# Performance work log

Measured on AMD Instinct MI355X. Metric: run time of the kernel, lower is better.

## Reference

```python
import jax, jax.numpy as jnp
import numpy as np

D_MODEL = 2048
NUM_CLASSES = 50257
N_BASIS = 8
RANK = 4
HIDDEN = 128
SCALE = 1.0
LN_EPS = 1e-5


def setup_inputs() -> dict:
    key = jax.random.key(0)
    ks = jax.random.split(key, 12)
    B = 2048
    lim_base = 1.0 / np.sqrt(D_MODEL)
    lim_ctx = 1.0 / np.sqrt(D_MODEL)
    lim_coeff = 1.0 / np.sqrt(HIDDEN)
    basis_std = np.sqrt(2.0 / (D_MODEL + RANK))
    return {
        "x": jax.random.normal(ks[0], (B, D_MODEL), jnp.float32),
        "context": jax.random.normal(ks[1], (B, D_MODEL), jnp.float32),
        "base_w": jax.random.uniform(ks[2], (NUM_CLASSES, D_MODEL), jnp.float32, -lim_base, lim_base),
        "base_b": jax.random.uniform(ks[3], (NUM_CLASSES,), jnp.float32, -lim_base, lim_base),
        "ctx_w": jax.random.uniform(ks[4], (HIDDEN, D_MODEL), jnp.float32, -lim_ctx, lim_ctx),
        "ctx_b": jax.random.uniform(ks[5], (HIDDEN,), jnp.float32, -lim_ctx, lim_ctx),
        "ln_g": jnp.ones((HIDDEN,), jnp.float32),
        "ln_b": jnp.zeros((HIDDEN,), jnp.float32),
        "coeff_w": jax.random.uniform(ks[6], (N_BASIS, HIDDEN), jnp.float32, -lim_coeff, lim_coeff),
        "coeff_b": jax.random.uniform(ks[7], (N_BASIS,), jnp.float32, -lim_coeff, lim_coeff),
        "basis_A": jax.random.normal(ks[8], (N_BASIS, RANK, D_MODEL), jnp.float32) * basis_std,
        # original zero-inits basis_B; use small randn so the LoRA path is exercised
        "basis_B": jax.random.normal(ks[9], (N_BASIS, NUM_CLASSES, RANK), jnp.float32) * 0.02,
    }


def reference(x, context, base_w, base_b, ctx_w, ctx_b, ln_g, ln_b,
              coeff_w, coeff_b, basis_A, basis_B):
    # ctx MLP: linear -> LayerNorm -> GELU(exact) -> linear
    h0 = context @ ctx_w.T + ctx_b                       # (B, H)
    mu = jnp.mean(h0, axis=-1, keepdims=True)
    var = jnp.var(h0, axis=-1, keepdims=True)
    hn = (h0 - mu) * jax.lax.rsqrt(var + LN_EPS) * ln_g + ln_b
    h = jax.nn.gelu(hn, approximate=False)
    coeffs = h @ coeff_w.T + coeff_b                     # (B, n_basis)

    # per-sample LoRA without materializing (B, num_classes, rank) B-tensor
    # z_br = x_bd * (coeffs_bn basis_A_nrd)
    z = jnp.einsum('bd,bn,nrd->br', x, coeffs, basis_A)  # (B, rank)
    # delta_bc = z_br * (coeffs_bn basis_B_ncr)
    u = jnp.einsum('bn,br->bnr', coeffs, z).reshape(x.shape[0], N_BASIS * RANK)
    Bmat = jnp.transpose(basis_B, (0, 2, 1)).reshape(N_BASIS * RANK, NUM_CLASSES)
    delta = u @ Bmat                                     # (B, num_classes)

    return x @ base_w.T + base_b + SCALE * delta
```

## Files before the change

kernel.cpp:

```cpp
#include <hip/hip_runtime.h>
#include <cstdint>
#include <cstddef>

#define D_MODEL 2048
#define NUM_CLASSES 50257
#define N_PAD 50304
#define N_BASIS 8
#define RANK 4
#define HIDDEN 128
#define B_ROWS 2048
#define KE 2080
#define NTILES 6288
#define LN_EPS 1e-5f

typedef short short8 __attribute__((ext_vector_type(8)));
typedef float f32x4 __attribute__((ext_vector_type(4)));

__device__ __forceinline__ uint16_t f2bf(float f) {
    union { float f; uint32_t u; } c; c.f = f;
    uint32_t r = c.u + 0x7FFFu + ((c.u >> 16) & 1u);
    return (uint16_t)(r >> 16);
}

__device__ __forceinline__ short8 pack8(float4 a, float4 b) {
    union { short8 v; uint16_t u[8]; } p;
    p.u[0] = f2bf(a.x); p.u[1] = f2bf(a.y); p.u[2] = f2bf(a.z); p.u[3] = f2bf(a.w);
    p.u[4] = f2bf(b.x); p.u[5] = f2bf(b.y); p.u[6] = f2bf(b.z); p.u[7] = f2bf(b.w);
    return p.v;
}

__device__ __forceinline__ short8 zero8() {
    union { short8 s; uint16_t u[8]; } z;
    #pragma unroll
    for (int i = 0; i < 8; i++) z.u[i] = 0;
    return z.s;
}

__device__ __forceinline__ void async16(const void* g, void* l) {
    __builtin_amdgcn_global_load_lds(
        (const __attribute__((address_space(1))) unsigned int*)g,
        (__attribute__((address_space(3))) unsigned int*)l, 16, 0, 0);
}

__global__ void k_cvt_x(const float* __restrict__ x, uint16_t* __restrict__ Aext) {
    int chunk = blockIdx.x * 256 + threadIdx.x;
    int b = chunk >> 8, c8 = (chunk & 255) * 8;
    const float4* src = (const float4*)(x + (size_t)b * D_MODEL + c8);
    float4 f0 = src[0], f1 = src[1];
    *(short8*)(Aext + (size_t)b * KE + c8) = pack8(f0, f1);
}

__global__ void k_transpose(const float* __restrict__ src, float* __restrict__ dst,
                            int R, int C) {
    int i = blockIdx.x * 256 + threadIdx.x;
    if (i >= R * C) return;
    int c = i / R, r = i - c * R;
    dst[i] = src[(size_t)r * C + c];
}

__global__ void k_cvt_bw(const float* __restrict__ bw, const float* __restrict__ bB,
                         uint16_t* __restrict__ Bext) {
    int row = blockIdx.x;
    int c8 = threadIdx.x * 8;
    short8 v;
    if (row < NUM_CLASSES) {
        const float4* src = (const float4*)(bw + (size_t)row * D_MODEL + c8);
        v = pack8(src[0], src[1]);
    } else v = zero8();
    *(short8*)(Bext + (size_t)row * KE + c8) = v;
    if (threadIdx.x < 4) {
        int t = threadIdx.x;
        short8 e;
        if (row < NUM_CLASSES) {
            float4 v0 = *(const float4*)(bB + ((size_t)(2 * t)     * NUM_CLASSES + row) * RANK);
            float4 v1 = *(const float4*)(bB + ((size_t)(2 * t + 1) * NUM_CLASSES + row) * RANK);
            e = pack8(v0, v1);
        } else e = zero8();
        *(short8*)(Bext + (size_t)row * KE + D_MODEL + t * 8) = e;
    }
}

__global__ void k_cvt_bbt(const float* __restrict__ bB, uint16_t* __restrict__ dst,
                          int ld, int coloff) {
    int row = blockIdx.x * 256 + threadIdx.x;
    if (row >= N_PAD) return;
    union { short8 v[4]; uint16_t u[32]; } p;
    if (row < NUM_CLASSES) {
        #pragma unroll
        for (int nb = 0; nb < N_BASIS; nb++) {
            float4 v = *(const float4*)(bB + ((size_t)nb * NUM_CLASSES + row) * RANK);
            p.u[nb*4+0] = f2bf(v.x); p.u[nb*4+1] = f2bf(v.y);
            p.u[nb*4+2] = f2bf(v.z); p.u[nb*4+3] = f2bf(v.w);
        }
    } else {
        #pragma unroll
        for (int i = 0; i < 32; i++) p.u[i] = 0;
    }
    uint16_t* d = dst + (size_t)row * ld + coloff;
    #pragma unroll
    for (int i = 0; i < 4; i++) *(short8*)(d + i * 8) = p.v[i];
}

__global__ void k_ctx(const float* __restrict__ context, const float* __restrict__ ctx_wT,
                      const float* __restrict__ ctx_b, const float* __restrict__ ln_g,
                      const float* __restrict__ ln_b, const float* __restrict__ coeff_w,
                      const float* __restrict__ coeff_b, float* __restrict__ coeffs) {
    __shared__ float sctx[D_MODEL];
    __shared__ float s1[HIDDEN], s2[HIDDEN], sh[HIDDEN];
    int tid = threadIdx.x, b = blockIdx.x;
    const float4* csrc = (const float4*)(context + (size_t)b * D_MODEL);
    for (int i = tid; i < D_MODEL / 4; i += HIDDEN) ((float4*)sctx)[i] = csrc[i];
    __syncthreads();
    float a0 = 0.f, a1 = 0.f, a2 = 0.f, a3 = 0.f;
    #pragma unroll 4
    for (int k = 0; k < D_MODEL; k += 4) {
        a0 += ctx_wT[(size_t)(k + 0) * HIDDEN + tid] * sctx[k + 0];
        a1 += ctx_wT[(size_t)(k + 1) * HIDDEN + tid] * sctx[k + 1];
        a2 += ctx_wT[(size_t)(k + 2) * HIDDEN + tid] * sctx[k + 2];
        a3 += ctx_wT[(size_t)(k + 3) * HIDDEN + tid] * sctx[k + 3];
    }
    float h0 = (a0 + a1) + (a2 + a3) + ctx_b[tid];
    s1[tid] = h0; s2[tid] = h0 * h0;
    __syncthreads();
    for (int off = HIDDEN / 2; off > 0; off >>= 1) {
        if (tid < off) { s1[tid] += s1[tid + off]; s2[tid] += s2[tid + off]; }
        __syncthreads();
    }
    float mu  = s1[0] * (1.f / HIDDEN);
    float var = s2[0] * (1.f / HIDDEN) - mu * mu;
    float hn = (h0 - mu) * rsqrtf(var + LN_EPS) * ln_g[tid] + ln_b[tid];
    float h = 0.5f * hn * (1.f + erff(hn * 0.70710678118654752f));
    sh[tid] = h;
    __syncthreads();
    if (tid < N_BASIS) {
        const float* cw = coeff_w + tid * HIDDEN;
        float a = 0.f;
        #pragma unroll 4
        for (int k = 0; k < HIDDEN; k++) a += cw[k] * sh[k];
        coeffs[b * N_BASIS + tid] = a + coeff_b[tid];
    }
}

__global__ void k_zu(const float* __restrict__ x, const float* __restrict__ basis_AT,
                     const float* __restrict__ coeffs, uint16_t* __restrict__ Aext) {
    __shared__ float sx[D_MODEL];
    __shared__ float part[128];
    __shared__ float st[32];
    __shared__ float sz[RANK];
    int tid = threadIdx.x, b = blockIdx.x;
    const float4* xs = (const float4*)(x + (size_t)b * D_MODEL);
    for (int i = tid; i < D_MODEL / 4; i += 128) ((float4*)sx)[i] = xs[i];
    __syncthreads();
    int j = tid & 31, s = tid >> 5;
    int k0 = s * (D_MODEL / 4);
    float a0 = 0.f, a1 = 0.f, a2 = 0.f, a3 = 0.f;
    #pragma unroll 4
    for (int k = 0; k < D_MODEL / 4; k += 4) {
        a0 += basis_AT[(size_t)(k0 + k + 0) * 32 + j] * sx[k0 + k + 0];
        a1 += basis_AT[(size_t)(k0 + k + 1) * 32 + j] * sx[k0 + k + 1];
        a2 += basis_AT[(size_t)(k0 + k + 2) * 32 + j] * sx[k0 + k + 2];
        a3 += basis_AT[(size_t)(k0 + k + 3) * 32 + j] * sx[k0 + k + 3];
    }
    part[tid] = (a0 + a1) + (a2 + a3);
    __syncthreads();
    if (tid < 32) st[tid] = part[tid] + part[tid + 32] + part[tid + 64] + part[tid + 96];
    __syncthreads();
    if (tid < RANK) {
        float z = 0.f;
        #pragma unroll
        for (int nb = 0; nb < N_BASIS; nb++) z += coeffs[b * N_BASIS + nb] * st[nb * RANK + tid];
        sz[tid] = z;
    }
    __syncthreads();
    if (tid < 32) {
        int nb = tid >> 2, r = tid & 3;
        float u = coeffs[b * N_BASIS + nb] * sz[r];
        Aext[(size_t)b * KE + D_MODEL + tid] = f2bf(u);
    }
}

template<bool FULLB>
__global__ __launch_bounds__(256) void k_gemm(
        const uint16_t* __restrict__ Aext,
        const uint16_t* __restrict__ Bbuf,
        const float* __restrict__ bw,
        const float* __restrict__ base_b,
        float* __restrict__ out) {
    __shared__ uint16_t sA[2][128 * 32];
    __shared__ uint16_t sB[2][128 * 32];
    const int tid = threadIdx.x;
    const int lane = tid & 63, w = tid >> 6;
    const int l = blockIdx.x;
    const int tile = (l & 7) * (NTILES / 8) + (l >> 3);
    const int bm = tile & 15, bn = tile >> 4;
    const int wm = (w >> 1) * 64, wn = (w & 1) * 64;
    const int sr = tid >> 2, sc = (tid & 3) * 8;
    f32x4 acc[4][4] = {};

    const uint16_t* gA = Aext + (size_t)(bm * 128 + sr) * KE + sc;

    auto stageA = [&](int kk, int sel) {
        async16(gA + kk, &sA[sel][w * 512]);
        async16(gA + (size_t)64 * KE + kk, &sA[sel][2048 + w * 512]);
    };
    auto stageBfull = [&](int kk, int sel) {
        const uint16_t* gB = Bbuf + (size_t)(bn * 128 + sr) * KE + sc + kk;
        async16(gB, &sB[sel][w * 512]);
        async16(gB + (size_t)64 * KE, &sB[sel][2048 + w * 512]);
    };
    auto stageBfb = [&](int kk, int sel) {
        if (kk < D_MODEL) {
            #pragma unroll
            for (int it = 0; it < 2; it++) {
                int rr = it * 64 + sr;
                int gr = bn * 128 + rr;
                short8 v;
                if (gr < NUM_CLASSES) {
                    const float4* src = (const float4*)(bw + (size_t)gr * D_MODEL + kk + sc);
                    v = pack8(src[0], src[1]);
                } else v = zero8();
                *(short8*)(&sB[sel][rr * 32 + sc]) = v;
            }
        } else {
            #pragma unroll
            for (int it = 0; it < 2; it++) {
                int rr = it * 64 + sr;
                async16(Bbuf + (size_t)(bn * 128 + rr) * 32 + (kk - D_MODEL) + sc,
                        &sB[sel][it * 2048 + w * 512]);
            }
        }
    };

    stageA(0, 0);
    if constexpr (FULLB) stageBfull(0, 0); else stageBfb(0, 0);
    __syncthreads();

    int cur = 0;
    for (int kk = 0; kk < KE; kk += 32) {
        int nxt = cur ^ 1;
        if (kk + 32 < KE) {
            stageA(kk + 32, nxt);
            if constexpr (FULLB) stageBfull(kk + 32, nxt); else stageBfb(kk + 32, nxt);
        }
        const uint16_t* pA = sA[cur] + (lane >> 4) * 8;
        const uint16_t* pB = sB[cur] + (lane >> 4) * 8;
        short8 af[4], bfv[4];
        #pragma unroll
        for (int i = 0; i < 4; i++)
            af[i] = *(const short8*)(pA + (wm + i * 16 + (lane & 15)) * 32);
        #pragma unroll
        for (int j = 0; j < 4; j++)
            bfv[j] = *(const short8*)(pB + (wn + j * 16 + (lane & 15)) * 32);
        #pragma unroll
        for (int i = 0; i < 4; i++)
            #pragma unroll
            for (int j = 0; j < 4; j++)
                acc[i][j] = __builtin_amdgcn_mfma_f32_16x16x32_bf16(af[i], bfv[j], acc[i][j], 0, 0, 0);
        __syncthreads();
        cur = nxt;
    }

    const int rb = bm * 128 + wm + ((lane >> 4) << 2);
    const int cb = bn * 128 + wn + (lane & 15);
    #pragma unroll
    for (int j = 0; j < 4; j++) {
        int col = cb + j * 16;
        if (col < NUM_CLASSES) {
            float bias = base_b[col];
            #pragma unroll
            for (int i = 0; i < 4; i++) {
                int r0 = rb + i * 16;
                out[(size_t)(r0 + 0) * NUM_CLASSES + col] = acc[i][j][0] + bias;
                out[(size_t)(r0 + 1) * NUM_CLASSES + col] = acc[i][j][1] + bias;
                out[(size_t)(r0 + 2) * NUM_CLASSES + col] = acc[i][j][2] + bias;
                out[(size_t)(r0 + 3) * NUM_CLASSES + col] = acc[i][j][3] + bias;
            }
        }
    }
}

extern "C" void kernel_launch(void* const* d_in, const int* in_sizes, int n_in,
                              void* d_out, int out_size, void* d_ws, size_t ws_size,
                              hipStream_t stream) {
    const float* x       = (const float*)d_in[0];
    const float* context = (const float*)d_in[1];
    const float* base_w  = (const float*)d_in[2];
    const float* base_b  = (const float*)d_in[3];
    const float* ctx_w   = (const float*)d_in[4];
    const float* ctx_b   = (const float*)d_in[5];
    const float* ln_g    = (const float*)d_in[6];
    const float* ln_b    = (const float*)d_in[7];
    const float* coeff_w = (const float*)d_in[8];
    const float* coeff_b = (const float*)d_in[9];
    const float* basis_A = (const float*)d_in[10];
    const float* basis_B = (const float*)d_in[11];
    float* out = (float*)d_out;

    uint8_t* ws = (uint8_t*)d_ws;
    const size_t szA    = (size_t)B_ROWS * KE * 2;
    const size_t szCoef = (size_t)B_ROWS * N_BASIS * 4;
    const size_t szWT   = (size_t)D_MODEL * HIDDEN * 4;
    const size_t szAT   = (size_t)D_MODEL * 32 * 4;
    const size_t szBext = (size_t)N_PAD * KE * 2;
    const size_t base   = szA + szCoef + szWT + szAT;
    const bool full = ws_size >= base + szBext;

    uint16_t* Aext    = (uint16_t*)ws;
    float*    coeffs  = (float*)(ws + szA);
    float*    ctx_wT  = (float*)(ws + szA + szCoef);
    float*    basisAT = (float*)(ws + szA + szCoef + szWT);
    uint16_t* Bbuf    = (uint16_t*)(ws + base);

    k_cvt_x<<<2048, 256, 0, stream>>>(x, Aext);
    k_transpose<<<(HIDDEN * D_MODEL + 255) / 256, 256, 0, stream>>>(ctx_w, ctx_wT, HIDDEN, D_MODEL);
    k_transpose<<<(32 * D_MODEL + 255) / 256, 256, 0, stream>>>(basis_A, basisAT, 32, D_MODEL);
    if (full) {
        k_cvt_bw<<<N_PAD, 256, 0, stream>>>(base_w, basis_B, Bbuf);
    } else {
        k_cvt_bbt<<<(N_PAD + 255) / 256, 256, 0, stream>>>(basis_B, Bbuf, 32, 0);
    }
    k_ctx<<<2048, HIDDEN, 0, stream>>>(context, ctx_wT, ctx_b, ln_g, ln_b,
                                       coeff_w, coeff_b, coeffs);
    k_zu<<<2048, 128, 0, stream>>>(x, basisAT, coeffs, Aext);

    if (full) k_gemm<true ><<<NTILES, 256, 0, stream>>>(Aext, Bbuf, base_w, base_b, out);
    else      k_gemm<false><<<NTILES, 256, 0, stream>>>(Aext, Bbuf, base_w, base_b, out);
}
```

Before: 1.529 ms.

## Add 256x256-tile GEMM with swizzled LDS, 64-wide K steps and deeper prefetch

```diff
diff --git a/kernel.cpp b/kernel.cpp
--- a/kernel.cpp
+++ b/kernel.cpp
@@ -5,12 +5,17 @@
 #define D_MODEL 2048
 #define NUM_CLASSES 50257
 #define N_PAD 50304
+#define N_PAD2 50432
 #define N_BASIS 8
 #define RANK 4
 #define HIDDEN 128
 #define B_ROWS 2048
 #define KE 2080
+#define KP 2112
+#define KPB (KP*2)
+#define NTK 33
 #define NTILES 6288
+#define NT2 1576
 #define LN_EPS 1e-5f
 
 typedef short short8 __attribute__((ext_vector_type(8)));
@@ -42,12 +47,20 @@
         (__attribute__((address_space(3))) unsigned int*)l, 16, 0, 0);
 }
 
+__device__ __forceinline__ int swz(int q) { return q ^ (((q >> 9) & 1) << 5); }
+
+#define BARRIER() do { asm volatile("" ::: "memory"); \
+    __builtin_amdgcn_s_barrier(); asm volatile("" ::: "memory"); } while (0)
+
 __global__ void k_cvt_x(const float* __restrict__ x, uint16_t* __restrict__ Aext) {
     int chunk = blockIdx.x * 256 + threadIdx.x;
-    int b = chunk >> 8, c8 = (chunk & 255) * 8;
-    const float4* src = (const float4*)(x + (size_t)b * D_MODEL + c8);
-    float4 f0 = src[0], f1 = src[1];
-    *(short8*)(Aext + (size_t)b * KE + c8) = pack8(f0, f1);
+    int b = chunk / 264, c8 = (chunk - b * 264) * 8;
+    short8 v;
+    if (c8 < D_MODEL) {
+        const float4* src = (const float4*)(x + (size_t)b * D_MODEL + c8);
+        v = pack8(src[0], src[1]);
+    } else v = zero8();
+    *(short8*)(Aext + (size_t)b * KP + c8) = v;
 }
 
 __global__ void k_transpose(const float* __restrict__ src, float* __restrict__ dst,
@@ -62,21 +75,22 @@
                          uint16_t* __restrict__ Bext) {
     int row = blockIdx.x;
     int c8 = threadIdx.x * 8;
+    bool valid = row < NUM_CLASSES;
     short8 v;
-    if (row < NUM_CLASSES) {
+    if (valid) {
         const float4* src = (const float4*)(bw + (size_t)row * D_MODEL + c8);
         v = pack8(src[0], src[1]);
     } else v = zero8();
-    *(short8*)(Bext + (size_t)row * KE + c8) = v;
-    if (threadIdx.x < 4) {
+    *(short8*)(Bext + (size_t)row * KP + c8) = v;
+    if (threadIdx.x < 8) {
         int t = threadIdx.x;
-        short8 e;
-        if (row < NUM_CLASSES) {
-            float4 v0 = *(const float4*)(bB + ((size_t)(2 * t)     * NUM_CLASSES + row) * RANK);
-            float4 v1 = *(const float4*)(bB + ((size_t)(2 * t + 1) * NUM_CLASSES + row) * RANK);
+        short8 e = zero8();
+        if (valid && t < 4) {
+            float4 v0 = *(const float4*)(bB + ((size_t)(2*t)   * NUM_CLASSES + row) * RANK);
+            float4 v1 = *(const float4*)(bB + ((size_t)(2*t+1) * NUM_CLASSES + row) * RANK);
             e = pack8(v0, v1);
-        } else e = zero8();
-        *(short8*)(Bext + (size_t)row * KE + D_MODEL + t * 8) = e;
+        }
+        *(short8*)(Bext + (size_t)row * KP + D_MODEL + t * 8) = e;
     }
 }
 
@@ -175,14 +189,150 @@
     if (tid < 32) {
         int nb = tid >> 2, r = tid & 3;
         float u = coeffs[b * N_BASIS + nb] * sz[r];
-        Aext[(size_t)b * KE + D_MODEL + tid] = f2bf(u);
-    }
-}
-
-template<bool FULLB>
-__global__ __launch_bounds__(256) void k_gemm(
+        Aext[(size_t)b * KP + D_MODEL + tid] = f2bf(u);
+    }
+}
+
+#define MMA_BLOCK(IG) do {                                                      \
+    __builtin_amdgcn_s_setprio(1);                                              \
+    _Pragma("unroll")                                                           \
+    for (int t = 0; t < 4; t++) {                                               \
+        _Pragma("unroll")                                                       \
+        for (int jj = 0; jj < 4; jj++)                                          \
+            acc[(IG)*4 + t][jj] = __builtin_amdgcn_mfma_f32_16x16x32_bf16(      \
+                af[t], bf[jj], acc[(IG)*4 + t][jj], 0, 0, 0);                   \
+    }                                                                           \
+    __builtin_amdgcn_s_setprio(0);                                              \
+} while (0)
+
+__global__ __launch_bounds__(512, 2) void k_gemm256(
         const uint16_t* __restrict__ Aext,
-        const uint16_t* __restrict__ Bbuf,
+        const uint16_t* __restrict__ Bext,
+        const float* __restrict__ base_b,
+        float* __restrict__ out) {
+    __shared__ __align__(16) uint16_t sA[2][2][8192];
+    __shared__ __align__(16) uint16_t sB[2][2][8192];
+    const int tid = threadIdx.x;
+    const int lane = tid & 63, w = tid >> 6;
+    const int wm = w >> 2, wn = w & 3;
+    const int bm = blockIdx.x & 7, bn = blockIdx.x >> 3;
+
+    int aoff[2][4], boff[4];
+    #pragma unroll
+    for (int ig = 0; ig < 2; ig++)
+        #pragma unroll
+        for (int t = 0; t < 4; t++) {
+            int r = wm * 128 + (ig * 4 + t) * 16 + (lane & 15);
+            aoff[ig][t] = swz(r * 64 + (lane >> 4) * 16);
+        }
+    #pragma unroll
+    for (int j = 0; j < 4; j++) {
+        int n = wn * 64 + j * 16 + (lane & 15);
+        boff[j] = swz(n * 64 + (lane >> 4) * 16);
+    }
+
+    const uint8_t* Aeb = (const uint8_t*)Aext;
+    const uint8_t* Beb = (const uint8_t*)Bext;
+    const int p0 = w * 1024 + lane * 16, p1 = p0 + 8192;
+    const int q0 = swz(p0), q1 = swz(p1);
+    const uint8_t* gA0 = Aeb + (size_t)(bm * 256 + (q0 >> 6)) * KPB + (q0 & 63);
+    const uint8_t* gA1 = Aeb + (size_t)(bm * 256 + (q1 >> 6)) * KPB + (q1 & 63);
+    const uint8_t* gB0 = Beb + (size_t)(bn * 256 + (q0 >> 6)) * KPB + (q0 & 63);
+    const uint8_t* gB1 = Beb + (size_t)(bn * 256 + (q1 >> 6)) * KPB + (q1 & 63);
+    uint8_t* sAb = (uint8_t*)sA;
+    uint8_t* sBb = (uint8_t*)sB;
+    const int ldst = w * 1024;
+
+    auto stA = [&](int T, int kh) {
+        uint8_t* d = sAb + (T & 1) * 32768 + kh * 16384;
+        int co = T * 128 + kh * 64;
+        async16(gA0 + co, d + ldst);
+        async16(gA1 + co, d + 8192 + ldst);
+    };
+    auto stB = [&](int T, int kh) {
+        uint8_t* d = sBb + (T & 1) * 32768 + kh * 16384;
+        int co = T * 128 + kh * 64;
+        async16(gB0 + co, d + ldst);
+        async16(gB1 + co, d + 8192 + ldst);
+    };
+
+    f32x4 acc[8][4] = {};
+    short8 af[4], bf[4];
+
+    stB(0, 0); stA(0, 0); stB(0, 1); stA(0, 1);
+    stB(1, 0); stA(1, 0); stB(1, 1);
+    asm volatile("s_waitcnt vmcnt(6)" ::: "memory");
+    BARRIER();
+
+    #pragma unroll 1
+    for (int a = 0; a < NTK; ++a) {
+        const int slot = a & 1;
+        const uint8_t* hA0 = sAb + slot * 32768;
+        const uint8_t* hA1 = hA0 + 16384;
+        const uint8_t* hB0 = sBb + slot * 32768;
+        const uint8_t* hB1 = hB0 + 16384;
+
+        #pragma unroll
+        for (int t = 0; t < 4; t++) af[t] = *(const short8*)(hA0 + aoff[0][t]);
+        #pragma unroll
+        for (int j = 0; j < 4; j++) bf[j] = *(const short8*)(hB0 + boff[j]);
+        if (a + 1 < NTK) stA(a + 1, 1);
+        BARRIER();
+        asm volatile("s_waitcnt lgkmcnt(0)" ::: "memory");
+        MMA_BLOCK(0);
+        BARRIER();
+
+        #pragma unroll
+        for (int t = 0; t < 4; t++) af[t] = *(const short8*)(hA0 + aoff[1][t]);
+        if (a + 2 < NTK) stB(a + 2, 0);
+        BARRIER();
+        asm volatile("s_waitcnt lgkmcnt(0)" ::: "memory");
+        MMA_BLOCK(1);
+        BARRIER();
+
+        #pragma unroll
+        for (int t = 0; t < 4; t++) af[t] = *(const short8*)(hA1 + aoff[0][t]);
+        #pragma unroll
+        for (int j = 0; j < 4; j++) bf[j] = *(const short8*)(hB1 + boff[j]);
+        if (a + 2 < NTK) stA(a + 2, 0);
+        BARRIER();
+        asm volatile("s_waitcnt lgkmcnt(0)" ::: "memory");
+        MMA_BLOCK(0);
+        BARRIER();
+
+        #pragma unroll
+        for (int t = 0; t < 4; t++) af[t] = *(const short8*)(hA1 + aoff[1][t]);
+        if (a + 2 < NTK) stB(a + 2, 1);
+        if (a < NTK - 2) asm volatile("s_waitcnt vmcnt(6)" ::: "memory");
+        else             asm volatile("s_waitcnt vmcnt(0)" ::: "memory");
+        BARRIER();
+        asm volatile("s_waitcnt lgkmcnt(0)" ::: "memory");
+        MMA_BLOCK(1);
+        BARRIER();
+    }
+
+    const int rb = bm * 256 + wm * 128 + ((lane >> 4) << 2);
+    const int cb = bn * 256 + wn * 64 + (lane & 15);
+    #pragma unroll
+    for (int j = 0; j < 4; j++) {
+        int col = cb + j * 16;
+        if (col < NUM_CLASSES) {
+            float bias = base_b[col];
+            #pragma unroll
+            for (int i = 0; i < 8; i++) {
+                int r0 = rb + i * 16;
+                out[(size_t)(r0 + 0) * NUM_CLASSES + col] = acc[i][j][0] + bias;
+                out[(size_t)(r0 + 1) * NUM_CLASSES + col] = acc[i][j][1] + bias;
+                out[(size_t)(r0 + 2) * NUM_CLASSES + col] = acc[i][j][2] + bias;
+                out[(size_t)(r0 + 3) * NUM_CLASSES + col] = acc[i][j][3] + bias;
+            }
+        }
+    }
+}
+
+__global__ __launch_bounds__(256) void k_gemm128(
+        const uint16_t* __restrict__ Aext,
+        const uint16_t* __restrict__ Bbt,
         const float* __restrict__ bw,
         const float* __restrict__ base_b,
         float* __restrict__ out) {
@@ -197,18 +347,13 @@
     const int sr = tid >> 2, sc = (tid & 3) * 8;
     f32x4 acc[4][4] = {};
 
-    const uint16_t* gA = Aext + (size_t)(bm * 128 + sr) * KE + sc;
+    const uint16_t* gA = Aext + (size_t)(bm * 128 + sr) * KP + sc;
 
     auto stageA = [&](int kk, int sel) {
         async16(gA + kk, &sA[sel][w * 512]);
-        async16(gA + (size_t)64 * KE + kk, &sA[sel][2048 + w * 512]);
+        async16(gA + (size_t)64 * KP + kk, &sA[sel][2048 + w * 512]);
     };
-    auto stageBfull = [&](int kk, int sel) {
-        const uint16_t* gB = Bbuf + (size_t)(bn * 128 + sr) * KE + sc + kk;
-        async16(gB, &sB[sel][w * 512]);
-        async16(gB + (size_t)64 * KE, &sB[sel][2048 + w * 512]);
-    };
-    auto stageBfb = [&](int kk, int sel) {
+    auto stageB = [&](int kk, int sel) {
         if (kk < D_MODEL) {
             #pragma unroll
             for (int it = 0; it < 2; it++) {
@@ -225,32 +370,25 @@
             #pragma unroll
             for (int it = 0; it < 2; it++) {
                 int rr = it * 64 + sr;
-                async16(Bbuf + (size_t)(bn * 128 + rr) * 32 + (kk - D_MODEL) + sc,
+                async16(Bbt + (size_t)(bn * 128 + rr) * 32 + (kk - D_MODEL) + sc,
                         &sB[sel][it * 2048 + w * 512]);
             }
         }
     };
 
-    stageA(0, 0);
-    if constexpr (FULLB) stageBfull(0, 0); else stageBfb(0, 0);
-    __syncthreads();
-
+    stageA(0, 0); stageB(0, 0);
+    __syncthreads();
     int cur = 0;
     for (int kk = 0; kk < KE; kk += 32) {
         int nxt = cur ^ 1;
-        if (kk + 32 < KE) {
-            stageA(kk + 32, nxt);
-            if constexpr (FULLB) stageBfull(kk + 32, nxt); else stageBfb(kk + 32, nxt);
-        }
-        const uint16_t* pA = sA[cur] + (lane >> 4) * 8;
-        const uint16_t* pB = sB[cur] + (lane >> 4) * 8;
+        if (kk + 32 < KE) { stageA(kk + 32, nxt); stageB(kk + 32, nxt); }
         short8 af[4], bfv[4];
         #pragma unroll
         for (int i = 0; i < 4; i++)
-            af[i] = *(const short8*)(pA + (wm + i * 16 + (lane & 15)) * 32);
+            af[i] = *(const short8*)(&sA[cur][(wm + i * 16 + (lane & 15)) * 32] + (lane >> 4) * 8);
         #pragma unroll
         for (int j = 0; j < 4; j++)
-            bfv[j] = *(const short8*)(pB + (wn + j * 16 + (lane & 15)) * 32);
+            bfv[j] = *(const short8*)(&sB[cur][(wn + j * 16 + (lane & 15)) * 32] + (lane >> 4) * 8);
         #pragma unroll
         for (int i = 0; i < 4; i++)
             #pragma unroll
@@ -297,11 +435,12 @@
     float* out = (float*)d_out;
 
     uint8_t* ws = (uint8_t*)d_ws;
-    const size_t szA    = (size_t)B_ROWS * KE * 2;
+    const size_t szA    = (size_t)B_ROWS * KP * 2;
     const size_t szCoef = (size_t)B_ROWS * N_BASIS * 4;
     const size_t szWT   = (size_t)D_MODEL * HIDDEN * 4;
     const size_t szAT   = (size_t)D_MODEL * 32 * 4;
-    const size_t szBext = (size_t)N_PAD * KE * 2;
+    const size_t szBext = (size_t)N_PAD2 * KP * 2;
+    const size_t szBbt  = (size_t)N_PAD * 32 * 2;
     const size_t base   = szA + szCoef + szWT + szAT;
     const bool full = ws_size >= base + szBext;
 
@@ -311,11 +450,11 @@
     float*    basisAT = (float*)(ws + szA + szCoef + szWT);
     uint16_t* Bbuf    = (uint16_t*)(ws + base);
 
-    k_cvt_x<<<2048, 256, 0, stream>>>(x, Aext);
+    k_cvt_x<<<2112, 256, 0, stream>>>(x, Aext);
     k_transpose<<<(HIDDEN * D_MODEL + 255) / 256, 256, 0, stream>>>(ctx_w, ctx_wT, HIDDEN, D_MODEL);
     k_transpose<<<(32 * D_MODEL + 255) / 256, 256, 0, stream>>>(basis_A, basisAT, 32, D_MODEL);
     if (full) {
-        k_cvt_bw<<<N_PAD, 256, 0, stream>>>(base_w, basis_B, Bbuf);
+        k_cvt_bw<<<N_PAD2, 256, 0, stream>>>(base_w, basis_B, Bbuf);
     } else {
         k_cvt_bbt<<<(N_PAD + 255) / 256, 256, 0, stream>>>(basis_B, Bbuf, 32, 0);
     }
@@ -323,6 +462,6 @@
                                        coeff_w, coeff_b, coeffs);
     k_zu<<<2048, 128, 0, stream>>>(x, basisAT, coeffs, Aext);
 
-    if (full) k_gemm<true ><<<NTILES, 256, 0, stream>>>(Aext, Bbuf, base_w, base_b, out);
-    else      k_gemm<false><<<NTILES, 256, 0, stream>>>(Aext, Bbuf, base_w, base_b, out);
-}
+    if (full) k_gemm256<<<NT2, 512, 0, stream>>>(Aext, Bbuf, base_b, out);
+    else      k_gemm128<<<NTILES, 256, 0, stream>>>(Aext, Bbuf, base_w, base_b, out);
+}
```

Measured after the change: 1.477 ms. -3.4%, faster.
